# Optimization experiments

Hardware: AMD Instinct MI355X
Metric: run time of the kernel (lower is better)

The kernel has to match this reference:

```python
import jax, jax.numpy as jnp
import numpy as np
from jax import lax

B, L, V, H = 2, 1024, 32000, 1024
EXP = 2; INNER = H * EXP; S = 16; DT = 64; K = 4
F_FFN = 2048; E = 8; TOPK = 2; EPS = 1e-5


def setup_inputs() -> dict:
    key = jax.random.key(0)
    ks = jax.random.split(key, 12)
    def nrm(k, shape, s=0.02):
        return jax.random.normal(k, shape, jnp.float32) * s
    inp = {}
    inp["input_ids"] = jax.random.randint(ks[0], (B, L), 0, V)
    inp["emb"] = nrm(ks[1], (V, H))
    inp["norm0_w"] = jnp.ones((H,), jnp.float32)
    inp["in_proj_w"] = nrm(ks[2], (2 * INNER, H))
    inp["conv_w"] = nrm(ks[3], (INNER, 1, K), 0.1)
    inp["conv_b"] = jnp.zeros((INNER,), jnp.float32)
    inp["x_proj_w"] = nrm(ks[4], (DT + 2 * S, INNER))
    inp["dt_proj_w"] = nrm(ks[5], (INNER, DT), 0.05)
    inp["dt_proj_b"] = jnp.full((INNER,), -2.0, jnp.float32)
    inp["a_log"] = jnp.log(jnp.broadcast_to(jnp.arange(1, S + 1, dtype=jnp.float32), (INNER, S)))
    inp["d_param"] = jnp.ones((INNER,), jnp.float32)
    inp["out_proj_w"] = nrm(ks[6], (H, INNER))
    inp["norm1_w"] = jnp.ones((H,), jnp.float32)
    inp["router_w"] = nrm(ks[7], (E, H))
    inp["router_b"] = jnp.zeros((E,), jnp.float32)
    inp["fc1_w"] = nrm(ks[8], (E, 2 * F_FFN, H))
    inp["fc2_w"] = nrm(ks[9], (E, H, F_FFN))
    inp["final_norm_w"] = jnp.ones((H,), jnp.float32)
    return inp


def _rms(x, w):
    return (x * lax.rsqrt(jnp.mean(x * x, -1, keepdims=True) + EPS)) * w


def _mamba_scan(u, delta, a_log, b, c, d):
    # u, delta: [B,L,INNER]; b, c: [B,L,S]; a_log: [INNER,S]; d: [INNER]
    a = -jnp.exp(a_log)
    dl = jax.nn.softplus(delta)
    def step(st, inp):
        u_t, d_t, b_t, c_t = inp  # [B,INNER], [B,INNER], [B,S], [B,S]
        st = jnp.exp(d_t[:, :, None] * a[None]) * st + (d_t * u_t)[:, :, None] * b_t[:, None, :]
        y = jnp.sum(st * c_t[:, None, :], -1) + u_t * d
        return st, y
    st0 = jnp.zeros((u.shape[0], INNER, S), jnp.float32)
    tm = lambda x: jnp.swapaxes(x, 0, 1)  # time-major
    _, ys = lax.scan(step, st0, (tm(u), tm(dl), tm(b), tm(c)))
    return tm(ys)


def reference(input_ids, emb, norm0_w, in_proj_w, conv_w, conv_b, x_proj_w,
              dt_proj_w, dt_proj_b, a_log, d_param, out_proj_w, norm1_w,
              router_w, router_b, fc1_w, fc2_w, final_norm_w):
    x = emb[input_ids]  # [B,L,H]
    # ---- layer 0: Mamba mixer ----
    xn = _rms(x, norm0_w)
    proj = xn @ in_proj_w.T  # [B,L,2*INNER]
    u, gate = proj[..., :INNER], proj[..., INNER:]
    u_t = jnp.swapaxes(u, 1, 2)  # [B,INNER,L]
    uc = lax.conv_general_dilated(u_t, conv_w, (1,), [(K - 1, 0)],
                                  dimension_numbers=('NCH', 'OIH', 'NCH'),
                                  feature_group_count=INNER) + conv_b[None, :, None]
    u_conv = jax.nn.silu(jnp.swapaxes(uc, 1, 2))  # [B,L,INNER]
    xp = u_conv @ x_proj_w.T  # [B,L,DT+2S]
    dt, b, c = xp[..., :DT], xp[..., DT:DT + S], xp[..., DT + S:]
    delta = dt @ dt_proj_w.T + dt_proj_b
    y = _mamba_scan(u_conv, delta, a_log, b, c, d_param)
    x = x + (y * jax.nn.silu(gate)) @ out_proj_w.T
    # ---- layer 1: dense MoE (every expert over all tokens, as reference) ----
    xn = _rms(x, norm1_w)
    logits = xn @ router_w.T + router_b  # [B,L,E]
    probs = jax.nn.softmax(logits, -1)
    topk_s, topk_i = lax.top_k(probs, TOPK)
    scores = jnp.sum(jax.nn.one_hot(topk_i, E, dtype=x.dtype) * topk_s[..., None], axis=2)  # [B,L,E]
    h1 = jnp.einsum('blh,eoh->belo', xn, fc1_w)  # [B,E,L,2F]
    hidden = jax.nn.silu(h1[..., :F_FFN]) * h1[..., F_FFN:]
    eo = jnp.einsum('belf,ehf->belh', hidden, fc2_w)  # [B,E,L,H]
    x = x + jnp.einsum('belh,ble->blh', eo, scores)
    # ---- final norm + tied lm head ----
    x = _rms(x, final_norm_w)
    return x @ emb.T  # [B,L,V]
```

## Files before the change

### kernel.cpp

```cpp
#include <hip/hip_runtime.h>
#include <cstdint>

#define HD 1024
#define INNER 2048
#define NTOK 2048
#define SEQL 1024
#define SDIM 16
#define DTR 64
#define VDIM 32000
#define FFN 2048
#define EPSV 1e-5f
#define SLOT_CAP 5120
#define MAX_TILES 40
#define NCH 32
#define CLEN 32

typedef __attribute__((ext_vector_type(8))) short short8;
typedef __attribute__((ext_vector_type(4))) float f32x4;

__device__ __forceinline__ unsigned short f2bf(float f){
  unsigned int u = __float_as_uint(f);
  u += 0x7FFF + ((u >> 16) & 1);
  return (unsigned short)(u >> 16);
}
__device__ __forceinline__ float sigm(float x){ return 1.f/(1.f+__expf(-x)); }

__device__ __forceinline__ void gload16(const unsigned short* g, unsigned short* l){
  __builtin_amdgcn_global_load_lds(
    (const __attribute__((address_space(1))) unsigned int*)g,
    (__attribute__((address_space(3))) unsigned int*)l, 16, 0, 0);
}

__device__ __forceinline__ float block_sum(float v, float* sb){
  #pragma unroll
  for (int m=32;m>=1;m>>=1) v += __shfl_xor(v, m, 64);
  int lane = threadIdx.x & 63, w = threadIdx.x >> 6;
  if (lane==0) sb[w]=v;
  __syncthreads();
  float s = sb[0]+sb[1]+sb[2]+sb[3];
  __syncthreads();
  return s;
}

__global__ __launch_bounds__(256) void embed_rms_k(
  const int* __restrict__ ids, const float* __restrict__ emb,
  const float* __restrict__ n0w, float* __restrict__ x, float* __restrict__ xn)
{
  __shared__ float sb[4];
  int tok = blockIdx.x, t = threadIdx.x;
  int id = ids[tok];
  float4 v = *(const float4*)(emb + (size_t)id*HD + t*4);
  *(float4*)(x + (size_t)tok*HD + t*4) = v;
  float tot = block_sum(v.x*v.x+v.y*v.y+v.z*v.z+v.w*v.w, sb);
  float rs = rsqrtf(tot/(float)HD + EPSV);
  float4 w = *(const float4*)(n0w + t*4);
  float4 o; o.x=v.x*rs*w.x; o.y=v.y*rs*w.y; o.z=v.z*rs*w.z; o.w=v.w*rs*w.w;
  *(float4*)(xn + (size_t)tok*HD + t*4) = o;
}

template<int EPI>
__global__ __launch_bounds__(256) void gemm_f32k(
  const float* __restrict__ A, int lda,
  const float* __restrict__ B,
  float* __restrict__ C, int ldc,
  int N, int K, const float* __restrict__ bias)
{
  __shared__ float As[16][68];
  __shared__ float Bs[16][68];
  int m0 = blockIdx.y*64, n0 = blockIdx.x*64;
  int t = threadIdx.x, tm = t & 15, tn = t >> 4;
  float acc[4][4] = {};
  int srow = t >> 2, skq = (t & 3) * 4;
  const float* arow = A + (size_t)(m0 + srow)*lda + skq;
  int nrow = n0 + srow;
  const float* brow = B + (size_t)nrow*K + skq;
  bool bok = nrow < N;
  for (int k0 = 0; k0 < K; k0 += 16) {
    float4 a = *(const float4*)(arow + k0);
    float4 b = bok ? *(const float4*)(brow + k0) : make_float4(0.f,0.f,0.f,0.f);
    __syncthreads();
    As[skq+0][srow]=a.x; As[skq+1][srow]=a.y; As[skq+2][srow]=a.z; As[skq+3][srow]=a.w;
    Bs[skq+0][srow]=b.x; Bs[skq+1][srow]=b.y; Bs[skq+2][srow]=b.z; Bs[skq+3][srow]=b.w;
    __syncthreads();
    #pragma unroll
    for (int k=0;k<16;k++){
      const float4 av = *(const float4*)&As[k][tm*4];
      const float4 bv = *(const float4*)&Bs[k][tn*4];
      float am[4] = {av.x, av.y, av.z, av.w};
      float bn[4] = {bv.x, bv.y, bv.z, bv.w};
      #pragma unroll
      for (int i=0;i<4;i++)
        #pragma unroll
        for (int j=0;j<4;j++)
          acc[i][j] += am[i]*bn[j];
    }
  }
  #pragma unroll
  for (int i=0;i<4;i++){
    int row = m0 + tm*4 + i;
    #pragma unroll
    for (int j=0;j<4;j++){
      int col = n0 + tn*4 + j;
      if (col < N){
        float v = acc[i][j];
        if (EPI==1){ v += bias[col]; v = (v > 20.f) ? v : log1pf(expf(v)); }
        if (EPI==2){ v += C[(size_t)row*ldc + col]; }
        C[(size_t)row*ldc + col] = v;
      }
    }
  }
}

__global__ __launch_bounds__(256) void conv_silu_k(
  const float* __restrict__ proj, const float* __restrict__ cw,
  const float* __restrict__ cb, float* __restrict__ uc)
{
  int idx = blockIdx.x*256 + threadIdx.x;
  int c = idx & (INNER-1);
  int l = (idx >> 11) & (SEQL-1);
  int b = idx >> 21;
  float s = cb[c];
  #pragma unroll
  for (int k=0;k<4;k++){
    int ll = l + k - 3;
    if (ll >= 0) s += proj[(size_t)(b*SEQL + ll)*4096 + c] * cw[c*4+k];
  }
  uc[idx] = s * sigm(s);
}

__global__ __launch_bounds__(256) void scan_p1(
  const float* __restrict__ dl, const float* __restrict__ uc,
  const float* __restrict__ xp, const float* __restrict__ alog,
  float* __restrict__ locfin, float* __restrict__ Pst)
{
  int c = blockIdx.x*256 + threadIdx.x;
  int chunk = blockIdx.y, b = blockIdx.z;
  float a[SDIM];
  #pragma unroll
  for (int s=0;s<SDIM;s++) a[s] = -expf(alog[c*SDIM+s]);
  float st[SDIM] = {};
  float P[SDIM];
  #pragma unroll
  for (int s=0;s<SDIM;s++) P[s] = 1.f;
  size_t base = (size_t)b*SEQL + chunk*CLEN;
  #pragma unroll 2
  for (int l=0;l<CLEN;l++){
    size_t tix = base + l;
    float d = dl[tix*INNER + c];
    float u = uc[tix*INNER + c];
    const float* bc = xp + tix*96 + 64;
    float w = d*u;
    #pragma unroll
    for (int s=0;s<SDIM;s++){
      float p = __expf(d*a[s]);
      st[s] = p*st[s] + w*bc[s];
      P[s] *= p;
    }
  }
  size_t cb = (size_t)(b*NCH + chunk)*SDIM*INNER + c;
  #pragma unroll
  for (int s=0;s<SDIM;s++){
    locfin[cb + (size_t)s*INNER] = st[s];
    Pst[cb + (size_t)s*INNER] = P[s];
  }
}

__global__ __launch_bounds__(256) void scan_p2(
  const float* __restrict__ locfin, const float* __restrict__ Pst,
  float* __restrict__ initst)
{
  int c = blockIdx.x*256 + threadIdx.x;
  int s = blockIdx.y, b = blockIdx.z;
  float carry = 0.f;
  #pragma unroll 4
  for (int chunk=0; chunk<NCH; chunk++){
    size_t idx = ((size_t)(b*NCH + chunk)*SDIM + s)*INNER + c;
    initst[idx] = carry;
    carry = Pst[idx]*carry + locfin[idx];
  }
}

__global__ __launch_bounds__(256) void scan_p3(
  const float* __restrict__ dl, const float* __restrict__ uc,
  const float* __restrict__ xp, const float* __restrict__ alog,
  const float* __restrict__ dpar, const float* __restrict__ initst,
  float* __restrict__ y)
{
  int c = blockIdx.x*256 + threadIdx.x;
  int chunk = blockIdx.y, b = blockIdx.z;
  float a[SDIM], st[SDIM];
  #pragma unroll
  for (int s=0;s<SDIM;s++) a[s] = -expf(alog[c*SDIM+s]);
  size_t cb = (size_t)(b*NCH + chunk)*SDIM*INNER + c;
  #pragma unroll
  for (int s=0;s<SDIM;s++) st[s] = initst[cb + (size_t)s*INNER];
  float dv = dpar[c];
  size_t base = (size_t)b*SEQL + chunk*CLEN;
  #pragma unroll 2
  for (int l=0;l<CLEN;l++){
    size_t tix = base + l;
    float d = dl[tix*INNER + c];
    float u = uc[tix*INNER + c];
    const float* bc = xp + tix*96 + 64;
    float w = d*u, acc = 0.f;
    #pragma unroll
    for (int s=0;s<SDIM;s++){
      float p = __expf(d*a[s]);
      st[s] = p*st[s] + w*bc[s];
      acc += st[s]*bc[16+s];
    }
    y[tix*INNER + c] = acc + u*dv;
  }
}

__global__ __launch_bounds__(256) void ygate_k(
  const float* __restrict__ y, const float* __restrict__ proj, float* __restrict__ yg)
{
  int idx = blockIdx.x*256 + threadIdx.x;
  int c = idx & (INNER-1); int t_ = idx >> 11;
  float g = proj[(size_t)t_*4096 + 2048 + c];
  yg[idx] = y[idx] * g * sigm(g);
}

__global__ __launch_bounds__(256) void rms_router_k(
  const float* __restrict__ x, const float* __restrict__ n1w,
  const float* __restrict__ rw, const float* __restrict__ rb,
  unsigned short* __restrict__ xnbf, int* __restrict__ ti, float* __restrict__ ts)
{
  __shared__ float sb[4];
  __shared__ float sb8[8][4];
  int tok = blockIdx.x, t = threadIdx.x;
  float4 v = *(const float4*)(x + (size_t)tok*HD + t*4);
  float tot = block_sum(v.x*v.x+v.y*v.y+v.z*v.z+v.w*v.w, sb);
  float rs = rsqrtf(tot/(float)HD + EPSV);
  float4 w = *(const float4*)(n1w + t*4);
  float4 xv; xv.x=v.x*rs*w.x; xv.y=v.y*rs*w.y; xv.z=v.z*rs*w.z; xv.w=v.w*rs*w.w;
  ushort4 o; o.x=f2bf(xv.x); o.y=f2bf(xv.y); o.z=f2bf(xv.z); o.w=f2bf(xv.w);
  *(ushort4*)(xnbf + (size_t)tok*HD + t*4) = o;
  float pe[8];
  #pragma unroll
  for (int e=0;e<8;e++){
    const float4 r4 = *(const float4*)(rw + (size_t)e*HD + t*4);
    pe[e] = xv.x*r4.x + xv.y*r4.y + xv.z*r4.z + xv.w*r4.w;
  }
  int lane = t & 63, wv = t >> 6;
  #pragma unroll
  for (int e=0;e<8;e++){
    float s = pe[e];
    #pragma unroll
    for (int m=32;m>=1;m>>=1) s += __shfl_xor(s, m, 64);
    if (lane==0) sb8[e][wv] = s;
  }
  __syncthreads();
  if (t==0){
    float lg[8], mx = -1e30f;
    for (int e=0;e<8;e++){ lg[e] = sb8[e][0]+sb8[e][1]+sb8[e][2]+sb8[e][3] + rb[e]; mx = fmaxf(mx, lg[e]); }
    float ex[8], sum=0.f;
    for (int e=0;e<8;e++){ ex[e]=expf(lg[e]-mx); sum+=ex[e]; }
    float inv = 1.f/sum;
    int i0=0; float p0=-1.f;
    for (int e=0;e<8;e++){ float p=ex[e]*inv; if (p>p0){p0=p;i0=e;} }
    int i1=-1; float p1=-1.f;
    for (int e=0;e<8;e++){ if (e==i0) continue; float p=ex[e]*inv; if (p>p1){p1=p;i1=e;} }
    ti[2*tok]=i0; ti[2*tok+1]=i1; ts[2*tok]=p0; ts[2*tok+1]=p1;
  }
}

__global__ void route_build_k(const int* __restrict__ ti, const float* __restrict__ ts,
  int* __restrict__ slot_token, int* __restrict__ tok_slots, int* __restrict__ tile_expert)
{
  __shared__ int cnt[8], cur[8];
  int t = threadIdx.x;
  if (t < 8) cnt[t] = 0;
  __syncthreads();
  for (int tok = t; tok < NTOK; tok += 256){
    atomicAdd(&cnt[ti[2*tok]], 1);
    atomicAdd(&cnt[ti[2*tok+1]], 1);
  }
  __syncthreads();
  if (t == 0){
    int off = 0, tile = 0;
    for (int e=0;e<8;e++){
      cur[e] = off;
      int nt2 = (cnt[e] + 127) >> 7;
      for (int j=0;j<nt2;j++) tile_expert[tile++] = e;
      off += nt2 << 7;
    }
    while (tile < MAX_TILES) tile_expert[tile++] = -1;
  }
  __syncthreads();
  for (int i = t; i < SLOT_CAP; i += 256) slot_token[i] = -1;
  __syncthreads();
  for (int tok = t; tok < NTOK; tok += 256){
    #pragma unroll
    for (int j=0;j<2;j++){
      int e = ti[2*tok+j];
      int p = atomicAdd(&cur[e], 1);
      slot_token[p] = tok;
      tok_slots[2*tok+j] = p;
    }
  }
}

template<bool GATHER, bool EXPERT>
__global__ __launch_bounds__(256) void gemm_bf16k(
  const unsigned short* __restrict__ A, int lda,
  const int* __restrict__ slot_token,
  const float* __restrict__ B0, long long expert_stride,
  const int* __restrict__ tile_expert,
  float* __restrict__ C, int ldc, int K)
{
  int mt = blockIdx.y, nt = blockIdx.x;
  const float* Bp = B0;
  if (EXPERT){
    int e = tile_expert[mt];
    if (e < 0) return;
    Bp = B0 + (long long)e * expert_stride;
  }
  int m0 = mt*128, n0 = nt*128;
  __shared__ unsigned short As[128][40];
  __shared__ unsigned short Bs[128][40];
  int t = threadIdx.x;
  int w = t >> 6, lane = t & 63;
  int wm = (w >> 1) * 64, wn = (w & 1) * 64;
  int lr = lane & 15, quad = lane >> 4;
  f32x4 acc[4][4] = {};

  int arow = t >> 1;
  int ahalf = t & 1;
  const unsigned short* asrc = nullptr;
  bool avalid = true;
  if (GATHER){
    int tok = slot_token[m0 + arow];
    avalid = (tok >= 0);
    if (avalid) asrc = A + (size_t)tok * lda;
  } else {
    asrc = A + (size_t)(m0 + arow) * lda;
  }
  const float* bsrc = Bp + (size_t)(n0 + arow) * K;

  for (int k0 = 0; k0 < K; k0 += 32){
    uint4 av0 = make_uint4(0,0,0,0), av1 = make_uint4(0,0,0,0);
    if (avalid){
      const uint4* p = (const uint4*)(asrc + k0 + ahalf*16);
      av0 = p[0]; av1 = p[1];
    }
    const float4* q = (const float4*)(bsrc + k0 + ahalf*16);
    float4 b0 = q[0], b1 = q[1], b2 = q[2], b3 = q[3];
    uint4 w0, w1;
    w0.x = (uint32_t)f2bf(b0.x) | ((uint32_t)f2bf(b0.y)<<16);
    w0.y = (uint32_t)f2bf(b0.z) | ((uint32_t)f2bf(b0.w)<<16);
    w0.z = (uint32_t)f2bf(b1.x) | ((uint32_t)f2bf(b1.y)<<16);
    w0.w = (uint32_t)f2bf(b1.z) | ((uint32_t)f2bf(b1.w)<<16);
    w1.x = (uint32_t)f2bf(b2.x) | ((uint32_t)f2bf(b2.y)<<16);
    w1.y = (uint32_t)f2bf(b2.z) | ((uint32_t)f2bf(b2.w)<<16);
    w1.z = (uint32_t)f2bf(b3.x) | ((uint32_t)f2bf(b3.y)<<16);
    w1.w = (uint32_t)f2bf(b3.z) | ((uint32_t)f2bf(b3.w)<<16);
    __syncthreads();
    *(uint4*)&As[arow][ahalf*16]     = av0;
    *(uint4*)&As[arow][ahalf*16 + 8] = av1;
    *(uint4*)&Bs[arow][ahalf*16]     = w0;
    *(uint4*)&Bs[arow][ahalf*16 + 8] = w1;
    __syncthreads();
    short8 af[4], bf[4];
    #pragma unroll
    for (int mi=0;mi<4;mi++) af[mi] = *(const short8*)&As[wm + mi*16 + lr][quad*8];
    #pragma unroll
    for (int ni=0;ni<4;ni++) bf[ni] = *(const short8*)&Bs[wn + ni*16 + lr][quad*8];
    #pragma unroll
    for (int mi=0;mi<4;mi++)
      #pragma unroll
      for (int ni=0;ni<4;ni++)
        acc[mi][ni] = __builtin_amdgcn_mfma_f32_16x16x32_bf16(af[mi], bf[ni], acc[mi][ni], 0, 0, 0);
  }
  #pragma unroll
  for (int mi=0;mi<4;mi++){
    int rbase = m0 + wm + mi*16 + quad*4;
    #pragma unroll
    for (int ni=0;ni<4;ni++){
      int col = n0 + wn + ni*16 + lr;
      float* cp = C + (size_t)rbase*ldc + col;
      #pragma unroll
      for (int r=0;r<4;r++) cp[(size_t)r*ldc] = acc[mi][ni][r];
    }
  }
}

__global__ __launch_bounds__(256) void f2bf_arr_k(
  const float* __restrict__ in, unsigned short* __restrict__ out)
{
  size_t i = (size_t)(blockIdx.x*256 + threadIdx.x) * 8;
  const float4* p = (const float4*)(in + i);
  float4 a = p[0], b = p[1];
  ushort4 o0, o1;
  o0.x=f2bf(a.x); o0.y=f2bf(a.y); o0.z=f2bf(a.z); o0.w=f2bf(a.w);
  o1.x=f2bf(b.x); o1.y=f2bf(b.y); o1.z=f2bf(b.z); o1.w=f2bf(b.w);
  *(ushort4*)(out + i)     = o0;
  *(ushort4*)(out + i + 4) = o1;
}

__global__ __launch_bounds__(256) void lmhead_k(
  const unsigned short* __restrict__ A,
  const unsigned short* __restrict__ B,
  float* __restrict__ C)
{
  __shared__ __align__(16) unsigned short As0[128][32];
  __shared__ __align__(16) unsigned short Bs0[128][32];
  __shared__ __align__(16) unsigned short As1[128][32];
  __shared__ __align__(16) unsigned short Bs1[128][32];
  int orig = blockIdx.x;
  int swz = (orig & 7)*500 + (orig >> 3);
  int mt = swz & 15, nt = swz >> 4;
  int m0 = mt*128, n0 = nt*128;
  int t = threadIdx.x, w = t >> 6, lane = t & 63;
  int wm = (w >> 1) * 64, wn = (w & 1) * 64;
  int lr = lane & 15, quad = lane >> 4;

  int row0 = w*16 + (lane>>2);
  int koff = ((lane&3) ^ ((lane>>3)&3)) * 8;
  int p0 = (w*1024 + lane*16) >> 1;
  int p1 = p0 + 2048;
  const unsigned short* gA0 = A + (size_t)(m0 + row0)*HD + koff;
  const unsigned short* gA1 = gA0 + (size_t)64*HD;
  const unsigned short* gB0 = B + (size_t)(n0 + row0)*HD + koff;
  const unsigned short* gB1 = gB0 + (size_t)64*HD;

  int sq = (quad ^ ((lr>>1)&3)) * 8;

  f32x4 acc[4][4] = {};

#define STAGE(AS,BS,k0) \
    gload16(gA0 + (k0), &AS[0][0] + p0); \
    gload16(gA1 + (k0), &AS[0][0] + p1); \
    gload16(gB0 + (k0), &BS[0][0] + p0); \
    gload16(gB1 + (k0), &BS[0][0] + p1);

#define COMPUTE(AS,BS) { \
    short8 af[4], bf[4]; \
    _Pragma("unroll") \
    for (int mi=0;mi<4;mi++) af[mi] = *(const short8*)&AS[wm + mi*16 + lr][sq]; \
    _Pragma("unroll") \
    for (int ni=0;ni<4;ni++) bf[ni] = *(const short8*)&BS[wn + ni*16 + lr][sq]; \
    _Pragma("unroll") \
    for (int mi=0;mi<4;mi++) \
      _Pragma("unroll") \
      for (int ni=0;ni<4;ni++) \
        acc[mi][ni] = __builtin_amdgcn_mfma_f32_16x16x32_bf16(af[mi], bf[ni], acc[mi][ni], 0, 0, 0); }

  STAGE(As0,Bs0, 0);
  __syncthreads();
  for (int k0 = 0; k0 < HD; k0 += 64){
    STAGE(As1,Bs1, k0+32);
    COMPUTE(As0,Bs0);
    __syncthreads();
    if (k0 + 64 < HD) { STAGE(As0,Bs0, k0+64); }
    COMPUTE(As1,Bs1);
    __syncthreads();
  }
#undef STAGE
#undef COMPUTE

  #pragma unroll
  for (int mi=0;mi<4;mi++){
    int rbase = m0 + wm + mi*16 + quad*4;
    #pragma unroll
    for (int ni=0;ni<4;ni++){
      int col = n0 + wn + ni*16 + lr;
      float* cp = C + (size_t)rbase*VDIM + col;
      #pragma unroll
      for (int r=0;r<4;r++) cp[(size_t)r*VDIM] = acc[mi][ni][r];
    }
  }
}

__global__ __launch_bounds__(256) void silu_mul_k(
  const float* __restrict__ h1, unsigned short* __restrict__ hidden)
{
  int idx = blockIdx.x*256 + threadIdx.x;
  int f = idx & (FFN-1); int slot = idx >> 11;
  float a = h1[(size_t)slot*2*FFN + f];
  float b = h1[(size_t)slot*2*FFN + FFN + f];
  hidden[idx] = f2bf(a*sigm(a)*b);
}

__global__ __launch_bounds__(256) void combine_rms_k(
  const float* __restrict__ x, const float* __restrict__ eo,
  const int* __restrict__ tok_slots, const float* __restrict__ ts,
  const float* __restrict__ fw, unsigned short* __restrict__ xnf)
{
  __shared__ float sb[4];
  int tok = blockIdx.x, t = threadIdx.x;
  int p0 = tok_slots[2*tok], p1 = tok_slots[2*tok+1];
  float s0 = ts[2*tok], s1 = ts[2*tok+1];
  float4 v  = *(const float4*)(x  + (size_t)tok*HD + t*4);
  float4 e0 = *(const float4*)(eo + (size_t)p0*HD + t*4);
  float4 e1 = *(const float4*)(eo + (size_t)p1*HD + t*4);
  v.x += s0*e0.x + s1*e1.x;
  v.y += s0*e0.y + s1*e1.y;
  v.z += s0*e0.z + s1*e1.z;
  v.w += s0*e0.w + s1*e1.w;
  float tot = block_sum(v.x*v.x+v.y*v.y+v.z*v.z+v.w*v.w, sb);
  float rs = rsqrtf(tot/(float)HD + EPSV);
  float4 w = *(const float4*)(fw + t*4);
  ushort4 o;
  o.x=f2bf(v.x*rs*w.x); o.y=f2bf(v.y*rs*w.y); o.z=f2bf(v.z*rs*w.z); o.w=f2bf(v.w*rs*w.w);
  *(ushort4*)(xnf + (size_t)tok*HD + t*4) = o;
}

extern "C" void kernel_launch(void* const* d_in, const int* in_sizes, int n_in,
                              void* d_out, int out_size, void* d_ws, size_t ws_size,
                              hipStream_t stream)
{
  const int*   ids  = (const int*)  d_in[0];
  const float* emb  = (const float*)d_in[1];
  const float* n0w  = (const float*)d_in[2];
  const float* ipw  = (const float*)d_in[3];
  const float* cw   = (const float*)d_in[4];
  const float* cb   = (const float*)d_in[5];
  const float* xpw  = (const float*)d_in[6];
  const float* dtw  = (const float*)d_in[7];
  const float* dtb  = (const float*)d_in[8];
  const float* alog = (const float*)d_in[9];
  const float* dpar = (const float*)d_in[10];
  const float* opw  = (const float*)d_in[11];
  const float* n1w  = (const float*)d_in[12];
  const float* rw   = (const float*)d_in[13];
  const float* rb   = (const float*)d_in[14];
  const float* f1w  = (const float*)d_in[15];
  const float* f2w  = (const float*)d_in[16];
  const float* fnw  = (const float*)d_in[17];
  float* out = (float*)d_out;
  char* ws = (char*)d_ws;

  size_t o_x       = 0;
  size_t o_xnbf    = o_x + 8388608;
  size_t o_ti      = o_xnbf + 4194304;
  size_t o_ts      = o_ti + 16384;
  size_t o_slott   = o_ts + 16384;
  size_t o_tslots  = o_slott + 20480;
  size_t o_tile    = o_tslots + 16384;
  size_t o_xn      = o_tile + 256;
  size_t o_proj    = o_xn + 8388608;
  size_t o_uconv   = o_proj + 33554432;
  size_t o_xp      = o_uconv + 16777216;
  size_t o_dl      = o_xp + 786432;
  size_t o_y       = o_dl + 16777216;
  size_t o_yg      = o_y + 16777216;
  size_t o_h1      = o_proj;
  size_t o_hidden  = o_yg + 16777216;
  size_t o_eo      = o_hidden + 20971520;
  size_t o_xnf     = o_eo + 20971520;
  size_t o_locfin  = o_hidden;
  size_t o_pst     = o_locfin + 8388608;
  size_t o_init    = o_pst + 8388608;
  size_t o_embbf   = o_proj;

  float* x      = (float*)(ws + o_x);
  unsigned short* xnbf = (unsigned short*)(ws + o_xnbf);
  int*   ti     = (int*)(ws + o_ti);
  float* ts     = (float*)(ws + o_ts);
  int*   slott  = (int*)(ws + o_slott);
  int*   tslots = (int*)(ws + o_tslots);
  int*   tile_e = (int*)(ws + o_tile);
  float* xn     = (float*)(ws + o_xn);
  float* proj   = (float*)(ws + o_proj);
  float* uconv  = (float*)(ws + o_uconv);
  float* xp     = (float*)(ws + o_xp);
  float* dl     = (float*)(ws + o_dl);
  float* y      = (float*)(ws + o_y);
  float* yg     = (float*)(ws + o_yg);
  float* h1     = (float*)(ws + o_h1);
  unsigned short* hidden = (unsigned short*)(ws + o_hidden);
  float* eo     = (float*)(ws + o_eo);
  unsigned short* xnf = (unsigned short*)(ws + o_xnf);
  float* locfin = (float*)(ws + o_locfin);
  float* pst    = (float*)(ws + o_pst);
  float* initst = (float*)(ws + o_init);
  unsigned short* embbf = (unsigned short*)(ws + o_embbf);

  embed_rms_k<<<NTOK,256,0,stream>>>(ids, emb, n0w, x, xn);
  gemm_f32k<0><<<dim3(64,32),256,0,stream>>>(xn, HD, ipw, proj, 4096, 4096, HD, nullptr);
  conv_silu_k<<<(NTOK*INNER)/256,256,0,stream>>>(proj, cw, cb, uconv);
  gemm_f32k<0><<<dim3(2,32),256,0,stream>>>(uconv, INNER, xpw, xp, 96, 96, INNER, nullptr);
  gemm_f32k<1><<<dim3(32,32),256,0,stream>>>(xp, 96, dtw, dl, INNER, INNER, DTR, dtb);
  scan_p1<<<dim3(8,NCH,2),256,0,stream>>>(dl, uconv, xp, alog, locfin, pst);
  scan_p2<<<dim3(8,SDIM,2),256,0,stream>>>(locfin, pst, initst);
  scan_p3<<<dim3(8,NCH,2),256,0,stream>>>(dl, uconv, xp, alog, dpar, initst, y);
  ygate_k<<<(NTOK*INNER)/256,256,0,stream>>>(y, proj, yg);
  gemm_f32k<2><<<dim3(16,32),256,0,stream>>>(yg, INNER, opw, x, HD, HD, INNER, nullptr);
  rms_router_k<<<NTOK,256,0,stream>>>(x, n1w, rw, rb, xnbf, ti, ts);
  route_build_k<<<1,256,0,stream>>>(ti, ts, slott, tslots, tile_e);
  gemm_bf16k<true,true><<<dim3(32,MAX_TILES),256,0,stream>>>(
      xnbf, HD, slott, f1w, 4096LL*1024LL, tile_e, h1, 4096, HD);
  silu_mul_k<<<(SLOT_CAP*FFN)/256,256,0,stream>>>(h1, hidden);
  f2bf_arr_k<<<(VDIM*HD/8)/256,256,0,stream>>>(emb, embbf);
  gemm_bf16k<false,true><<<dim3(8,MAX_TILES),256,0,stream>>>(
      hidden, FFN, nullptr, f2w, 1024LL*2048LL, tile_e, eo, HD, FFN);
  combine_rms_k<<<NTOK,256,0,stream>>>(x, eo, tslots, ts, fnw, xnf);
  lmhead_k<<<4000,256,0,stream>>>(xnf, embbf, out);
}
```

Measured before the change: 1.428 ms.

## Run in_proj and out_proj GEMMs on MFMA with split-bf16 (3-pass) emulation

```diff
diff --git a/kernel.cpp b/kernel.cpp
--- a/kernel.cpp
+++ b/kernel.cpp
@@ -23,6 +23,13 @@
   u += 0x7FFF + ((u >> 16) & 1);
   return (unsigned short)(u >> 16);
 }
+__device__ __forceinline__ float bf2f(unsigned short h){
+  return __uint_as_float(((unsigned int)h) << 16);
+}
+__device__ __forceinline__ void splitbf(float v, unsigned short &h, unsigned short &l){
+  h = f2bf(v);
+  l = f2bf(v - bf2f(h));
+}
 __device__ __forceinline__ float sigm(float x){ return 1.f/(1.f+__expf(-x)); }
 
 __device__ __forceinline__ void gload16(const unsigned short* g, unsigned short* l){
@@ -44,7 +51,8 @@
 
 __global__ __launch_bounds__(256) void embed_rms_k(
   const int* __restrict__ ids, const float* __restrict__ emb,
-  const float* __restrict__ n0w, float* __restrict__ x, float* __restrict__ xn)
+  const float* __restrict__ n0w, float* __restrict__ x,
+  unsigned short* __restrict__ xnh, unsigned short* __restrict__ xnl)
 {
   __shared__ float sb[4];
   int tok = blockIdx.x, t = threadIdx.x;
@@ -55,7 +63,109 @@
   float rs = rsqrtf(tot/(float)HD + EPSV);
   float4 w = *(const float4*)(n0w + t*4);
   float4 o; o.x=v.x*rs*w.x; o.y=v.y*rs*w.y; o.z=v.z*rs*w.z; o.w=v.w*rs*w.w;
-  *(float4*)(xn + (size_t)tok*HD + t*4) = o;
+  ushort4 h, l;
+  splitbf(o.x, h.x, l.x); splitbf(o.y, h.y, l.y);
+  splitbf(o.z, h.z, l.z); splitbf(o.w, h.w, l.w);
+  *(ushort4*)(xnh + (size_t)tok*HD + t*4) = h;
+  *(ushort4*)(xnl + (size_t)tok*HD + t*4) = l;
+}
+
+__global__ __launch_bounds__(256) void split_bf_k(
+  const float* __restrict__ in, unsigned short* __restrict__ h, unsigned short* __restrict__ l)
+{
+  size_t i = (size_t)(blockIdx.x*256 + threadIdx.x) * 8;
+  const float4* p = (const float4*)(in + i);
+  float4 a = p[0], b = p[1];
+  ushort4 h0,l0,h1,l1;
+  splitbf(a.x,h0.x,l0.x); splitbf(a.y,h0.y,l0.y); splitbf(a.z,h0.z,l0.z); splitbf(a.w,h0.w,l0.w);
+  splitbf(b.x,h1.x,l1.x); splitbf(b.y,h1.y,l1.y); splitbf(b.z,h1.z,l1.z); splitbf(b.w,h1.w,l1.w);
+  *(ushort4*)(h + i)     = h0;
+  *(ushort4*)(h + i + 4) = h1;
+  *(ushort4*)(l + i)     = l0;
+  *(ushort4*)(l + i + 4) = l1;
+}
+
+template<int EPI>
+__global__ __launch_bounds__(256) void gemm_bfsplit_k(
+  const unsigned short* __restrict__ Ah, const unsigned short* __restrict__ Al,
+  const unsigned short* __restrict__ Bh, const unsigned short* __restrict__ Bl,
+  float* __restrict__ C, int ldc, int K)
+{
+  __shared__ __align__(16) unsigned short AH[2][128][32];
+  __shared__ __align__(16) unsigned short AL[2][128][32];
+  __shared__ __align__(16) unsigned short BH[2][128][32];
+  __shared__ __align__(16) unsigned short BL[2][128][32];
+  int mt = blockIdx.y, nt = blockIdx.x;
+  int m0 = mt*128, n0 = nt*128;
+  int t = threadIdx.x, w = t >> 6, lane = t & 63;
+  int wm = (w >> 1) * 64, wn = (w & 1) * 64;
+  int lr = lane & 15, quad = lane >> 4;
+  int row0 = w*16 + (lane>>2);
+  int koff = ((lane&3) ^ ((lane>>3)&3)) * 8;
+  int p0 = (w*1024 + lane*16) >> 1;
+  int p1 = p0 + 2048;
+  size_t a0 = (size_t)(m0 + row0)*K + koff;
+  size_t b0 = (size_t)(n0 + row0)*K + koff;
+  const unsigned short* gAh0 = Ah + a0; const unsigned short* gAh1 = gAh0 + (size_t)64*K;
+  const unsigned short* gAl0 = Al + a0; const unsigned short* gAl1 = gAl0 + (size_t)64*K;
+  const unsigned short* gBh0 = Bh + b0; const unsigned short* gBh1 = gBh0 + (size_t)64*K;
+  const unsigned short* gBl0 = Bl + b0; const unsigned short* gBl1 = gBl0 + (size_t)64*K;
+  int sq = (quad ^ ((lr>>1)&3)) * 8;
+
+  f32x4 acc[4][4] = {};
+
+#define STG(bi,k0) \
+    gload16(gAh0+(k0), &AH[bi][0][0]+p0); gload16(gAh1+(k0), &AH[bi][0][0]+p1); \
+    gload16(gAl0+(k0), &AL[bi][0][0]+p0); gload16(gAl1+(k0), &AL[bi][0][0]+p1); \
+    gload16(gBh0+(k0), &BH[bi][0][0]+p0); gload16(gBh1+(k0), &BH[bi][0][0]+p1); \
+    gload16(gBl0+(k0), &BL[bi][0][0]+p0); gload16(gBl1+(k0), &BL[bi][0][0]+p1);
+
+#define CMP(bi) { \
+    short8 ah[4], al[4], bh[4], bl[4]; \
+    _Pragma("unroll") \
+    for (int mi=0;mi<4;mi++){ \
+      ah[mi] = *(const short8*)&AH[bi][wm + mi*16 + lr][sq]; \
+      al[mi] = *(const short8*)&AL[bi][wm + mi*16 + lr][sq]; } \
+    _Pragma("unroll") \
+    for (int ni=0;ni<4;ni++){ \
+      bh[ni] = *(const short8*)&BH[bi][wn + ni*16 + lr][sq]; \
+      bl[ni] = *(const short8*)&BL[bi][wn + ni*16 + lr][sq]; } \
+    _Pragma("unroll") \
+    for (int mi=0;mi<4;mi++) \
+      _Pragma("unroll") \
+      for (int ni=0;ni<4;ni++){ \
+        acc[mi][ni] = __builtin_amdgcn_mfma_f32_16x16x32_bf16(al[mi], bh[ni], acc[mi][ni], 0, 0, 0); \
+        acc[mi][ni] = __builtin_amdgcn_mfma_f32_16x16x32_bf16(ah[mi], bl[ni], acc[mi][ni], 0, 0, 0); \
+        acc[mi][ni] = __builtin_amdgcn_mfma_f32_16x16x32_bf16(ah[mi], bh[ni], acc[mi][ni], 0, 0, 0); } }
+
+  STG(0, 0);
+  __syncthreads();
+  for (int k0 = 0; k0 < K; k0 += 64){
+    STG(1, k0+32);
+    CMP(0);
+    __syncthreads();
+    if (k0 + 64 < K) { STG(0, k0+64); }
+    CMP(1);
+    __syncthreads();
+  }
+#undef STG
+#undef CMP
+
+  #pragma unroll
+  for (int mi=0;mi<4;mi++){
+    int rbase = m0 + wm + mi*16 + quad*4;
+    #pragma unroll
+    for (int ni=0;ni<4;ni++){
+      int col = n0 + wn + ni*16 + lr;
+      float* cp = C + (size_t)rbase*ldc + col;
+      #pragma unroll
+      for (int r=0;r<4;r++){
+        float v = acc[mi][ni][r];
+        if (EPI==2) v += cp[(size_t)r*ldc];
+        cp[(size_t)r*ldc] = v;
+      }
+    }
+  }
 }
 
 template<int EPI>
@@ -214,12 +324,16 @@
 }
 
 __global__ __launch_bounds__(256) void ygate_k(
-  const float* __restrict__ y, const float* __restrict__ proj, float* __restrict__ yg)
+  const float* __restrict__ y, const float* __restrict__ proj,
+  unsigned short* __restrict__ ygh, unsigned short* __restrict__ ygl)
 {
   int idx = blockIdx.x*256 + threadIdx.x;
   int c = idx & (INNER-1); int t_ = idx >> 11;
   float g = proj[(size_t)t_*4096 + 2048 + c];
-  yg[idx] = y[idx] * g * sigm(g);
+  float v = y[idx] * g * sigm(g);
+  unsigned short h, l;
+  splitbf(v, h, l);
+  ygh[idx] = h; ygl[idx] = l;
 }
 
 __global__ __launch_bounds__(256) void rms_router_k(
@@ -554,6 +668,14 @@
   size_t o_pst     = o_locfin + 8388608;
   size_t o_init    = o_pst + 8388608;
   size_t o_embbf   = o_proj;
+  size_t o_xnh     = o_xn;
+  size_t o_xnl     = o_xn + 4194304;
+  size_t o_iph     = o_uconv;
+  size_t o_ipl     = o_uconv + 8388608;
+  size_t o_oph     = o_xn;
+  size_t o_opl     = o_xn + 4194304;
+  size_t o_ygh     = o_yg;
+  size_t o_ygl     = o_yg + 8388608;
 
   float* x      = (float*)(ws + o_x);
   unsigned short* xnbf = (unsigned short*)(ws + o_xnbf);
@@ -562,13 +684,11 @@
   int*   slott  = (int*)(ws + o_slott);
   int*   tslots = (int*)(ws + o_tslots);
   int*   tile_e = (int*)(ws + o_tile);
-  float* xn     = (float*)(ws + o_xn);
   float* proj   = (float*)(ws + o_proj);
   float* uconv  = (float*)(ws + o_uconv);
   float* xp     = (float*)(ws + o_xp);
   float* dl     = (float*)(ws + o_dl);
   float* y      = (float*)(ws + o_y);
-  float* yg     = (float*)(ws + o_yg);
   float* h1     = (float*)(ws + o_h1);
   unsigned short* hidden = (unsigned short*)(ws + o_hidden);
   float* eo     = (float*)(ws + o_eo);
@@ -577,17 +697,27 @@
   float* pst    = (float*)(ws + o_pst);
   float* initst = (float*)(ws + o_init);
   unsigned short* embbf = (unsigned short*)(ws + o_embbf);
-
-  embed_rms_k<<<NTOK,256,0,stream>>>(ids, emb, n0w, x, xn);
-  gemm_f32k<0><<<dim3(64,32),256,0,stream>>>(xn, HD, ipw, proj, 4096, 4096, HD, nullptr);
+  unsigned short* xnh = (unsigned short*)(ws + o_xnh);
+  unsigned short* xnl = (unsigned short*)(ws + o_xnl);
+  unsigned short* iph = (unsigned short*)(ws + o_iph);
+  unsigned short* ipl = (unsigned short*)(ws + o_ipl);
+  unsigned short* oph = (unsigned short*)(ws + o_oph);
+  unsigned short* opl = (unsigned short*)(ws + o_opl);
+  unsigned short* ygh = (unsigned short*)(ws + o_ygh);
+  unsigned short* ygl = (unsigned short*)(ws + o_ygl);
+
+  embed_rms_k<<<NTOK,256,0,stream>>>(ids, emb, n0w, x, xnh, xnl);
+  split_bf_k<<<(4096*1024/8)/256,256,0,stream>>>(ipw, iph, ipl);
+  gemm_bfsplit_k<0><<<dim3(32,16),256,0,stream>>>(xnh, xnl, iph, ipl, proj, 4096, HD);
   conv_silu_k<<<(NTOK*INNER)/256,256,0,stream>>>(proj, cw, cb, uconv);
+  split_bf_k<<<(1024*2048/8)/256,256,0,stream>>>(opw, oph, opl);
   gemm_f32k<0><<<dim3(2,32),256,0,stream>>>(uconv, INNER, xpw, xp, 96, 96, INNER, nullptr);
   gemm_f32k<1><<<dim3(32,32),256,0,stream>>>(xp, 96, dtw, dl, INNER, INNER, DTR, dtb);
   scan_p1<<<dim3(8,NCH,2),256,0,stream>>>(dl, uconv, xp, alog, locfin, pst);
   scan_p2<<<dim3(8,SDIM,2),256,0,stream>>>(locfin, pst, initst);
   scan_p3<<<dim3(8,NCH,2),256,0,stream>>>(dl, uconv, xp, alog, dpar, initst, y);
-  ygate_k<<<(NTOK*INNER)/256,256,0,stream>>>(y, proj, yg);
-  gemm_f32k<2><<<dim3(16,32),256,0,stream>>>(yg, INNER, opw, x, HD, HD, INNER, nullptr);
+  ygate_k<<<(NTOK*INNER)/256,256,0,stream>>>(y, proj, ygh, ygl);
+  gemm_bfsplit_k<2><<<dim3(8,16),256,0,stream>>>(ygh, ygl, oph, opl, x, HD, INNER);
   rms_router_k<<<NTOK,256,0,stream>>>(x, n1w, rw, rb, xnbf, ti, ts);
   route_build_k<<<1,256,0,stream>>>(ti, ts, slott, tslots, tile_e);
   gemm_bf16k<true,true><<<dim3(32,MAX_TILES),256,0,stream>>>(
```

New measurement: 1.224 ms. 14.3% less time.
